# Performance work log

Measured on AMD Instinct MI355X. Metric: run time of the kernel, lower is better.

The kernel has to match this reference:

```python
import jax, jax.numpy as jnp
import numpy as np

N = 300000
H = 700
W_GRID = 700
CIN = 64
COUT = 64
K = 9


def setup_inputs() -> dict:
    rng = np.random.default_rng(0)
    lin = rng.permutation(H * W_GRID)[:N]
    ys = (lin // W_GRID).astype(np.int64)
    xs = (lin % W_GRID).astype(np.int64)
    grid = np.full(H * W_GRID, -1, np.int32)
    grid[lin] = np.arange(N, dtype=np.int32)
    offs = [(dy, dx) for dy in (-1, 0, 1) for dx in (-1, 0, 1)]

    def build(d):
        nbr = np.full((K, N), -1, np.int32)
        for k, (dy, dx) in enumerate(offs):
            ny = ys + dy * d
            nx = xs + dx * d
            valid = (ny >= 0) & (ny < H) & (nx >= 0) & (nx < W_GRID)
            l = np.clip(ny * W_GRID + nx, 0, H * W_GRID - 1)
            nbr[k] = np.where(valid, grid[l], -1)
        return jnp.asarray(nbr)

    nbr_d1 = build(1)
    nbr_d2 = build(2)

    key = jax.random.key(0)
    ks = jax.random.split(key, 16)
    f32 = jnp.float32

    def bn(k, c):
        s = jax.random.uniform(k, (c,), f32, 0.5, 1.5)
        b = jax.random.normal(jax.random.fold_in(k, 1), (c,), f32) * 0.1
        return s, b

    features = jax.random.normal(ks[0], (N, CIN), f32)
    W1 = jax.random.normal(ks[1], (K, CIN, COUT), f32) * 0.05
    W2a = jax.random.normal(ks[2], (CIN, COUT // 2), f32) * 0.05
    W2b = jax.random.normal(ks[3], (K, COUT // 2, COUT), f32) * 0.05
    W3 = jax.random.normal(ks[4], (K, CIN, COUT), f32) * 0.05
    Wf = jax.random.normal(ks[5], (3 * COUT, COUT), f32) * 0.05
    A1_w = jax.random.normal(ks[6], (3 * COUT, COUT // 4), f32) * 0.1
    A1_b = jnp.zeros((COUT // 4,), f32)
    A2_w = jax.random.normal(ks[7], (COUT // 4, 3 * COUT), f32) * 0.1
    A2_b = jnp.zeros((3 * COUT,), f32)
    bn1_s, bn1_b = bn(ks[8], COUT)
    bn2a_s, bn2a_b = bn(ks[9], COUT // 2)
    bn2b_s, bn2b_b = bn(ks[10], COUT)
    bn3_s, bn3_b = bn(ks[11], COUT)
    bnf_s, bnf_b = bn(ks[12], COUT)

    return dict(features=features, W1=W1, bn1_s=bn1_s, bn1_b=bn1_b,
                W2a=W2a, bn2a_s=bn2a_s, bn2a_b=bn2a_b,
                W2b=W2b, bn2b_s=bn2b_s, bn2b_b=bn2b_b,
                W3=W3, bn3_s=bn3_s, bn3_b=bn3_b,
                A1_w=A1_w, A1_b=A1_b, A2_w=A2_w, A2_b=A2_b,
                Wf=Wf, bnf_s=bnf_s, bnf_b=bnf_b,
                nbr_d1=nbr_d1, nbr_d2=nbr_d2)


def _sconv(f, nbr, W):
    # f: [N, Cin], nbr: [K, N] (-1 = no neighbor), W: [K, Cin, Cout]
    mask = (nbr >= 0)[..., None]                      # [K, N, 1]
    g = jnp.where(mask, f[jnp.clip(nbr, 0)], 0.0)     # [K, N, Cin] gather
    return jnp.einsum('knc,kcd->nd', g, W)            # [N, Cout]


def _bnrelu(x, s, b):
    # inference-mode BatchNorm folded into affine scale/shift, then ReLU
    return jax.nn.relu(x * s + b)


def reference(features, W1, bn1_s, bn1_b, W2a, bn2a_s, bn2a_b, W2b, bn2b_s, bn2b_b,
              W3, bn3_s, bn3_b, A1_w, A1_b, A2_w, A2_b, Wf, bnf_s, bnf_b,
              nbr_d1, nbr_d2):
    # path 1: 3x3 sparse conv + BN + ReLU
    feat1 = _bnrelu(_sconv(features, nbr_d1, W1), bn1_s, bn1_b)
    # path 2: 1x1 bottleneck + 3x3 sparse conv
    h = _bnrelu(features @ W2a, bn2a_s, bn2a_b)
    feat2 = _bnrelu(_sconv(h, nbr_d1, W2b), bn2b_s, bn2b_b)
    # path 3: 3x3 dilated (d=2) sparse conv
    feat3 = _bnrelu(_sconv(features, nbr_d2, W3), bn3_s, bn3_b)
    ms = jnp.concatenate([feat1, feat2, feat3], axis=1)   # [N, 3*Cout]
    # SE-style attention from global max pool over active sites
    pooled = jnp.max(ms, axis=0)                          # [3*Cout]
    attn = jax.nn.sigmoid(jax.nn.relu(pooled @ A1_w + A1_b) @ A2_w + A2_b)
    ms = ms * attn
    # 1x1 fusion conv + BN + ReLU
    fused = _bnrelu(ms @ Wf, bnf_s, bnf_b)                # [N, Cout]
    return fused
```

## Files before the change

### kernel.cpp

```cpp
#include <hip/hip_runtime.h>

#define N_PTS 300000
#define NPAD  300032
#define ZROW  N_PTS

typedef _Float16 f16;
typedef _Float16 f16x8 __attribute__((ext_vector_type(8)));
typedef float    f32x4 __attribute__((ext_vector_type(4)));

__device__ __forceinline__ f16 f2h(float x) { return (f16)x; }

union u4f16 { uint4 u; f16x8 h; };

#define HEAD_BLOCKS (NPAD / 256)
#define WP_BLOCKS   368

__global__ __launch_bounds__(256) void k_head(
    const float* __restrict__ feat, const float* __restrict__ W2a,
    const float* __restrict__ s2a, const float* __restrict__ b2a,
    const float* __restrict__ W1, const float* __restrict__ W2b,
    const float* __restrict__ W3,
    f16* __restrict__ featf, f16* __restrict__ hf,
    f16* __restrict__ Wt1, f16* __restrict__ Wt2b, f16* __restrict__ Wt3)
{
    if (blockIdx.x >= HEAD_BLOCKS) {
        int j = (blockIdx.x - HEAD_BLOCKS) * 256 + threadIdx.x;
        if (j < 36864) {
            int k = j >> 12, rem = j & 4095, d = rem >> 6, c = rem & 63;
            Wt1[j] = f2h(W1[(k << 12) + (c << 6) + d]);
        } else if (j < 73728) {
            int jj = j - 36864;
            int k = jj >> 12, rem = jj & 4095, d = rem >> 6, c = rem & 63;
            Wt3[jj] = f2h(W3[(k << 12) + (c << 6) + d]);
        } else if (j < 73728 + 18432) {
            int jj = j - 73728;
            int k = jj >> 11, rem = jj & 2047, d = rem >> 5, c2 = rem & 31;
            Wt2b[jj] = f2h(W2b[k * 2048 + c2 * 64 + d]);
        }
        return;
    }

    int lane = threadIdx.x & 63, wave = threadIdx.x >> 6;
    int n0 = (blockIdx.x * 4 + wave) * 64;
    int ln = lane & 15, q = lane >> 4;

    f16x8 a[4][2];
#pragma unroll
    for (int mt = 0; mt < 4; mt++) {
        int n = n0 + mt * 16 + ln;
#pragma unroll
        for (int ks = 0; ks < 2; ks++) {
            u4f16 v;
            if (n < N_PTS) {
                const float* p = feat + (long)n * 64 + ks * 32 + q * 8;
                float4 lo = *(const float4*)p;
                float4 hi = *(const float4*)(p + 4);
                v.h[0] = f2h(lo.x); v.h[1] = f2h(lo.y);
                v.h[2] = f2h(lo.z); v.h[3] = f2h(lo.w);
                v.h[4] = f2h(hi.x); v.h[5] = f2h(hi.y);
                v.h[6] = f2h(hi.z); v.h[7] = f2h(hi.w);
            } else {
                v.u = make_uint4(0u, 0u, 0u, 0u);
            }
            a[mt][ks] = v.h;
            *(uint4*)(featf + (long)n * 64 + ks * 32 + q * 8) = v.u;
        }
    }

    f32x4 acc[4][2];
    for (int mt = 0; mt < 4; mt++) for (int nt = 0; nt < 2; nt++)
        acc[mt][nt] = (f32x4){0.f, 0.f, 0.f, 0.f};
#pragma unroll
    for (int ks = 0; ks < 2; ks++)
#pragma unroll
        for (int nt = 0; nt < 2; nt++) {
            f16x8 b;
#pragma unroll
            for (int j = 0; j < 8; j++)
                b[j] = f2h(W2a[(ks * 32 + q * 8 + j) * 32 + nt * 16 + ln]);
#pragma unroll
            for (int mt = 0; mt < 4; mt++)
                acc[mt][nt] = __builtin_amdgcn_mfma_f32_16x16x32_f16(a[mt][ks], b, acc[mt][nt], 0, 0, 0);
        }

#pragma unroll
    for (int nt = 0; nt < 2; nt++) {
        int ch = nt * 16 + ln;
        float s = s2a[ch], bb = b2a[ch];
#pragma unroll
        for (int mt = 0; mt < 4; mt++)
#pragma unroll
            for (int r = 0; r < 4; r++) {
                int n = n0 + mt * 16 + q * 4 + r;
                float v = (n < N_PTS) ? fmaxf(acc[mt][nt][r] * s + bb, 0.f) : 0.f;
                hf[(long)n * 32 + ch] = f2h(v);
            }
    }
}

template <int CIN>
__device__ __forceinline__ void loadrows(
    uint4 (&dst)[4][CIN / 32], const int (&idx)[4],
    const f16* __restrict__ src, int q)
{
#pragma unroll
    for (int mt = 0; mt < 4; mt++) {
        const f16* p = src + (long)idx[mt] * CIN + q * 8;
#pragma unroll
        for (int ks = 0; ks < CIN / 32; ks++)
            dst[mt][ks] = *(const uint4*)(p + ks * 32);
    }
}

__device__ __forceinline__ void loadidx(
    int (&dst)[4], const int* __restrict__ nbr, int k, int n0, int ln)
{
    const int* nb = nbr + k * N_PTS;
#pragma unroll
    for (int mt = 0; mt < 4; mt++) {
        int nn = n0 + mt * 16 + ln;
        int v = (nn < N_PTS) ? nb[nn] : -1;
        dst[mt] = (v < 0) ? ZROW : v;
    }
}

template <int CIN>
__device__ __forceinline__ void conv_path(
    const f16* __restrict__ src, const f16* __restrict__ Wt,
    const int* __restrict__ nbr,
    int lane, int n0,
    const float* __restrict__ bns, const float* __restrict__ bnb,
    f16* __restrict__ msf, int colBase, float* __restrict__ pooled)
{
    constexpr int KS = CIN / 32;
    int ln = lane & 15, q = lane >> 4;

    f32x4 acc[4][4];
    for (int mt = 0; mt < 4; mt++) for (int nt = 0; nt < 4; nt++)
        acc[mt][nt] = (f32x4){0.f, 0.f, 0.f, 0.f};

    int  idxr[4][4];
    uint4 raw[4][4][KS];

#pragma unroll
    for (int k = 0; k < 4; k++) loadidx(idxr[k], nbr, k, n0, ln);
#pragma unroll
    for (int k = 0; k < 3; k++) loadrows<CIN>(raw[k], idxr[k], src, q);

#pragma unroll
    for (int k = 0; k < 9; k++) {
        if (k + 3 < 9) loadrows<CIN>(raw[(k + 3) & 3], idxr[(k + 3) & 3], src, q);
        if (k + 4 < 9) loadidx(idxr[k & 3], nbr, k + 4, n0, ln);
        const f16* Wk = Wt + k * CIN * 64;
#pragma unroll
        for (int ks = 0; ks < KS; ks++)
#pragma unroll
            for (int nt = 0; nt < 4; nt++) {
                f16x8 b = *(const f16x8*)(Wk + ((nt * 16 + ln) * CIN + ks * 32 + q * 8));
#pragma unroll
                for (int mt = 0; mt < 4; mt++) {
                    u4f16 v; v.u = raw[k & 3][mt][ks];
                    acc[mt][nt] = __builtin_amdgcn_mfma_f32_16x16x32_f16(v.h, b, acc[mt][nt], 0, 0, 0);
                }
            }
    }

#pragma unroll
    for (int nt = 0; nt < 4; nt++) {
        int ch = colBase + nt * 16 + ln;
        float s = bns[nt * 16 + ln], bb = bnb[nt * 16 + ln];
        float cmax = 0.f;
#pragma unroll
        for (int mt = 0; mt < 4; mt++)
#pragma unroll
            for (int r = 0; r < 4; r++) {
                int n = n0 + mt * 16 + q * 4 + r;
                float v = fmaxf(acc[mt][nt][r] * s + bb, 0.f);
                msf[(long)n * 192 + ch] = f2h(v);
                if (n < N_PTS) cmax = fmaxf(cmax, v);
            }
        cmax = fmaxf(cmax, __shfl_xor(cmax, 16));
        cmax = fmaxf(cmax, __shfl_xor(cmax, 32));
        if (q == 0) atomicMax((int*)(pooled + ch), __float_as_int(cmax));
    }
}

__global__ __launch_bounds__(256, 2) void k_conv(
    const f16* __restrict__ featf, const f16* __restrict__ hf,
    const f16* __restrict__ Wt1, const f16* __restrict__ Wt2b, const f16* __restrict__ Wt3,
    const int* __restrict__ nbr1, const int* __restrict__ nbr2,
    const float* __restrict__ bn1_s, const float* __restrict__ bn1_b,
    const float* __restrict__ bn2b_s, const float* __restrict__ bn2b_b,
    const float* __restrict__ bn3_s, const float* __restrict__ bn3_b,
    f16* __restrict__ msf, float* __restrict__ pooled)
{
    int lane = threadIdx.x & 63, wave = threadIdx.x >> 6;
    int u = blockIdx.x * 4 + wave;
    int tile = u / 3, path = u - tile * 3;
    int n0 = tile * 64;
    if (path == 0)
        conv_path<64>(featf, Wt1,  nbr1, lane, n0, bn1_s,  bn1_b,  msf, 0,   pooled);
    else if (path == 1)
        conv_path<32>(hf,    Wt2b, nbr1, lane, n0, bn2b_s, bn2b_b, msf, 64,  pooled);
    else
        conv_path<64>(featf, Wt3,  nbr2, lane, n0, bn3_s,  bn3_b,  msf, 128, pooled);
}

__global__ __launch_bounds__(256) void k_attn(
    const float* __restrict__ pooled,
    const float* __restrict__ A1w, const float* __restrict__ A1b,
    const float* __restrict__ A2w, const float* __restrict__ A2b,
    const float* __restrict__ Wf, f16* __restrict__ Wfst)
{
    __shared__ float sp[192], sa1[16], sattn[192];
    int t = threadIdx.x;
    if (t < 192) sp[t] = pooled[t];
    __syncthreads();
    if (t < 16) {
        float acc = A1b[t];
        for (int i = 0; i < 192; i++) acc += sp[i] * A1w[i * 16 + t];
        sa1[t] = fmaxf(acc, 0.f);
    }
    __syncthreads();
    if (t < 192) {
        float acc = A2b[t];
        for (int i = 0; i < 16; i++) acc += sa1[i] * A2w[i * 192 + t];
        sattn[t] = 1.f / (1.f + expf(-acc));
    }
    __syncthreads();
    for (int i = t; i < 192 * 64; i += 256) {
        int d = i / 192, j = i % 192;
        Wfst[i] = f2h(Wf[j * 64 + d] * sattn[j]);
    }
}

__global__ __launch_bounds__(256, 4) void k_fuse(
    const f16* __restrict__ msf, const f16* __restrict__ Wfst,
    const float* __restrict__ sf, const float* __restrict__ bf_,
    float* __restrict__ out)
{
    int lane = threadIdx.x & 63, wave = threadIdx.x >> 6;
    int n0 = (blockIdx.x * 4 + wave) * 32;
    int ln = lane & 15, q = lane >> 4;

    uint4 araw[6][2];
#pragma unroll
    for (int kt = 0; kt < 6; kt++)
#pragma unroll
        for (int mt = 0; mt < 2; mt++)
            araw[kt][mt] = *(const uint4*)(msf + (long)(n0 + mt * 16 + ln) * 192 + kt * 32 + q * 8);

    f32x4 acc[2][4];
    for (int mt = 0; mt < 2; mt++) for (int nt = 0; nt < 4; nt++)
        acc[mt][nt] = (f32x4){0.f, 0.f, 0.f, 0.f};

#pragma unroll
    for (int kt = 0; kt < 6; kt++)
#pragma unroll
        for (int nt = 0; nt < 4; nt++) {
            f16x8 b = *(const f16x8*)(Wfst + ((nt * 16 + ln) * 192 + kt * 32 + q * 8));
#pragma unroll
            for (int mt = 0; mt < 2; mt++) {
                u4f16 v; v.u = araw[kt][mt];
                acc[mt][nt] = __builtin_amdgcn_mfma_f32_16x16x32_f16(v.h, b, acc[mt][nt], 0, 0, 0);
            }
        }

#pragma unroll
    for (int nt = 0; nt < 4; nt++) {
        int ch = nt * 16 + ln;
        float s = sf[ch], bb = bf_[ch];
#pragma unroll
        for (int mt = 0; mt < 2; mt++)
#pragma unroll
            for (int r = 0; r < 4; r++) {
                int n = n0 + mt * 16 + q * 4 + r;
                if (n < N_PTS)
                    out[(long)n * 64 + ch] = fmaxf(acc[mt][nt][r] * s + bb, 0.f);
            }
    }
}

extern "C" void kernel_launch(void* const* d_in, const int* in_sizes, int n_in,
                              void* d_out, int out_size, void* d_ws, size_t ws_size,
                              hipStream_t stream)
{
    const float* features = (const float*)d_in[0];
    const float* W1     = (const float*)d_in[1];
    const float* bn1_s  = (const float*)d_in[2];
    const float* bn1_b  = (const float*)d_in[3];
    const float* W2a    = (const float*)d_in[4];
    const float* bn2a_s = (const float*)d_in[5];
    const float* bn2a_b = (const float*)d_in[6];
    const float* W2b    = (const float*)d_in[7];
    const float* bn2b_s = (const float*)d_in[8];
    const float* bn2b_b = (const float*)d_in[9];
    const float* W3     = (const float*)d_in[10];
    const float* bn3_s  = (const float*)d_in[11];
    const float* bn3_b  = (const float*)d_in[12];
    const float* A1w    = (const float*)d_in[13];
    const float* A1b    = (const float*)d_in[14];
    const float* A2w    = (const float*)d_in[15];
    const float* A2b    = (const float*)d_in[16];
    const float* Wf     = (const float*)d_in[17];
    const float* bnf_s  = (const float*)d_in[18];
    const float* bnf_b  = (const float*)d_in[19];
    const int*   nbr1   = (const int*)d_in[20];
    const int*   nbr2   = (const int*)d_in[21];

    char* ws = (char*)d_ws;
    size_t off = 0;
    f16* featf = (f16*)(ws + off); off += (size_t)NPAD * 64 * 2;
    f16* hf    = (f16*)(ws + off); off += (size_t)NPAD * 32 * 2;
    f16* msf   = (f16*)(ws + off); off += (size_t)NPAD * 192 * 2;
    f16* Wt1   = (f16*)(ws + off); off += 9 * 64 * 64 * 2;
    f16* Wt3   = (f16*)(ws + off); off += 9 * 64 * 64 * 2;
    f16* Wt2b  = (f16*)(ws + off); off += 9 * 32 * 64 * 2;
    f16* Wfst  = (f16*)(ws + off); off += 192 * 64 * 2;
    float* pooled = (float*)(ws + off); off += 256 * 4;

    hipMemsetAsync(pooled, 0, 192 * sizeof(float), stream);

    k_head<<<HEAD_BLOCKS + WP_BLOCKS, 256, 0, stream>>>(
        features, W2a, bn2a_s, bn2a_b, W1, W2b, W3,
        featf, hf, Wt1, Wt2b, Wt3);
    k_conv<<<(NPAD / 64) * 3 / 4, 256, 0, stream>>>(featf, hf, Wt1, Wt2b, Wt3, nbr1, nbr2,
                                           bn1_s, bn1_b, bn2b_s, bn2b_b, bn3_s, bn3_b,
                                           msf, pooled);
    k_attn<<<1, 256, 0, stream>>>(pooled, A1w, A1b, A2w, A2b, Wf, Wfst);
    k_fuse<<<NPAD / 128, 256, 0, stream>>>(msf, Wfst, bnf_s, bnf_b, (float*)d_out);
}
```

Measured before the change: 483.1 us.

## Hold conv weights in registers, swap MFMA operands, bpermute neighbor indices

The conv path now loads all 9 taps of weight fragments into registers up front instead of reloading them from memory per tap. It swaps the MFMA operand order so output channels map to rows, which lets each lane write 4 packed fp16 values per point and reduce the pooled max with lane shuffles. Neighbor indices are loaded once per lane for all taps and spread across lanes with ds_bpermute, and the gather ring shrinks to 3 slots. The much higher register use forces launch bounds down to 1 block per SM, which lowers occupancy and risks spilling.

```diff
diff --git a/kernel.cpp b/kernel.cpp
--- a/kernel.cpp
+++ b/kernel.cpp
@@ -99,28 +99,17 @@
 }
 
 template <int CIN>
-__device__ __forceinline__ void loadrows(
-    uint4 (&dst)[4][CIN / 32], const int (&idx)[4],
-    const f16* __restrict__ src, int q)
-{
-#pragma unroll
-    for (int mt = 0; mt < 4; mt++) {
-        const f16* p = src + (long)idx[mt] * CIN + q * 8;
+__device__ __forceinline__ void fill_tap(
+    uint4 (&slot)[4][CIN / 32], int idxk,
+    const f16* __restrict__ src, int ln, int q)
+{
+#pragma unroll
+    for (int pg = 0; pg < 4; pg++) {
+        int rid = __builtin_amdgcn_ds_bpermute((pg * 16 + ln) * 4, idxk);
+        const f16* p = src + (long)rid * CIN + q * 8;
 #pragma unroll
         for (int ks = 0; ks < CIN / 32; ks++)
-            dst[mt][ks] = *(const uint4*)(p + ks * 32);
-    }
-}
-
-__device__ __forceinline__ void loadidx(
-    int (&dst)[4], const int* __restrict__ nbr, int k, int n0, int ln)
-{
-    const int* nb = nbr + k * N_PTS;
-#pragma unroll
-    for (int mt = 0; mt < 4; mt++) {
-        int nn = n0 + mt * 16 + ln;
-        int v = (nn < N_PTS) ? nb[nn] : -1;
-        dst[mt] = (v < 0) ? ZROW : v;
+            slot[pg][ks] = *(const uint4*)(p + ks * 32);
     }
 }
 
@@ -135,57 +124,80 @@
     constexpr int KS = CIN / 32;
     int ln = lane & 15, q = lane >> 4;
 
+    int idxf[9];
+#pragma unroll
+    for (int k = 0; k < 9; k++) {
+        int nn = n0 + lane;
+        int v = (nn < N_PTS) ? nbr[k * N_PTS + nn] : -1;
+        idxf[k] = (v < 0) ? ZROW : v;
+    }
+
+    f16x8 wfr[9][4][KS];
+#pragma unroll
+    for (int t = 0; t < 9; t++)
+#pragma unroll
+        for (int ct = 0; ct < 4; ct++)
+#pragma unroll
+            for (int ks = 0; ks < KS; ks++)
+                wfr[t][ct][ks] = *(const f16x8*)(Wt + (t * 64 + ct * 16 + ln) * CIN + ks * 32 + q * 8);
+
     f32x4 acc[4][4];
-    for (int mt = 0; mt < 4; mt++) for (int nt = 0; nt < 4; nt++)
-        acc[mt][nt] = (f32x4){0.f, 0.f, 0.f, 0.f};
-
-    int  idxr[4][4];
-    uint4 raw[4][4][KS];
-
-#pragma unroll
-    for (int k = 0; k < 4; k++) loadidx(idxr[k], nbr, k, n0, ln);
-#pragma unroll
-    for (int k = 0; k < 3; k++) loadrows<CIN>(raw[k], idxr[k], src, q);
+    for (int ct = 0; ct < 4; ct++) for (int pg = 0; pg < 4; pg++)
+        acc[ct][pg] = (f32x4){0.f, 0.f, 0.f, 0.f};
+
+    uint4 ring[3][4][KS];
+    fill_tap<CIN>(ring[0], idxf[0], src, ln, q);
+    fill_tap<CIN>(ring[1], idxf[1], src, ln, q);
+    fill_tap<CIN>(ring[2], idxf[2], src, ln, q);
 
 #pragma unroll
     for (int k = 0; k < 9; k++) {
-        if (k + 3 < 9) loadrows<CIN>(raw[(k + 3) & 3], idxr[(k + 3) & 3], src, q);
-        if (k + 4 < 9) loadidx(idxr[k & 3], nbr, k + 4, n0, ln);
-        const f16* Wk = Wt + k * CIN * 64;
+        const int s = k % 3;
 #pragma unroll
         for (int ks = 0; ks < KS; ks++)
 #pragma unroll
-            for (int nt = 0; nt < 4; nt++) {
-                f16x8 b = *(const f16x8*)(Wk + ((nt * 16 + ln) * CIN + ks * 32 + q * 8));
-#pragma unroll
-                for (int mt = 0; mt < 4; mt++) {
-                    u4f16 v; v.u = raw[k & 3][mt][ks];
-                    acc[mt][nt] = __builtin_amdgcn_mfma_f32_16x16x32_f16(v.h, b, acc[mt][nt], 0, 0, 0);
+            for (int ct = 0; ct < 4; ct++)
+#pragma unroll
+                for (int pg = 0; pg < 4; pg++) {
+                    u4f16 v; v.u = ring[s][pg][ks];
+                    acc[ct][pg] = __builtin_amdgcn_mfma_f32_16x16x32_f16(
+                        wfr[k][ct][ks], v.h, acc[ct][pg], 0, 0, 0);
                 }
-            }
-    }
-
-#pragma unroll
-    for (int nt = 0; nt < 4; nt++) {
-        int ch = colBase + nt * 16 + ln;
-        float s = bns[nt * 16 + ln], bb = bnb[nt * 16 + ln];
-        float cmax = 0.f;
-#pragma unroll
-        for (int mt = 0; mt < 4; mt++)
+        if (k + 3 < 9) fill_tap<CIN>(ring[s], idxf[k + 3], src, ln, q);
+    }
+
+#pragma unroll
+    for (int ct = 0; ct < 4; ct++) {
+        f32x4 sv = *(const f32x4*)(bns + ct * 16 + q * 4);
+        f32x4 bv = *(const f32x4*)(bnb + ct * 16 + q * 4);
+        float rmax[4] = {0.f, 0.f, 0.f, 0.f};
+#pragma unroll
+        for (int pg = 0; pg < 4; pg++) {
+            int pt = n0 + pg * 16 + ln;
+            bool valid = pt < N_PTS;
+            union { f16 h[4]; uint2 u2; } pk;
 #pragma unroll
             for (int r = 0; r < 4; r++) {
-                int n = n0 + mt * 16 + q * 4 + r;
-                float v = fmaxf(acc[mt][nt][r] * s + bb, 0.f);
-                msf[(long)n * 192 + ch] = f2h(v);
-                if (n < N_PTS) cmax = fmaxf(cmax, v);
-            }
-        cmax = fmaxf(cmax, __shfl_xor(cmax, 16));
-        cmax = fmaxf(cmax, __shfl_xor(cmax, 32));
-        if (q == 0) atomicMax((int*)(pooled + ch), __float_as_int(cmax));
-    }
-}
-
-__global__ __launch_bounds__(256, 2) void k_conv(
+                float v = fmaxf(acc[ct][pg][r] * sv[r] + bv[r], 0.f);
+                pk.h[r] = f2h(v);
+                if (valid) rmax[r] = fmaxf(rmax[r], v);
+            }
+            *(uint2*)(msf + (long)pt * 192 + colBase + ct * 16 + q * 4) = pk.u2;
+        }
+#pragma unroll
+        for (int r = 0; r < 4; r++) {
+            float m = rmax[r];
+            m = fmaxf(m, __shfl_xor(m, 1));
+            m = fmaxf(m, __shfl_xor(m, 2));
+            m = fmaxf(m, __shfl_xor(m, 4));
+            m = fmaxf(m, __shfl_xor(m, 8));
+            if (ln == 0)
+                atomicMax((int*)(pooled + colBase + ct * 16 + q * 4 + r), __float_as_int(m));
+        }
+    }
+}
+
+__global__ __launch_bounds__(256, 1) void k_conv(
     const f16* __restrict__ featf, const f16* __restrict__ hf,
     const f16* __restrict__ Wt1, const f16* __restrict__ Wt2b, const f16* __restrict__ Wt3,
     const int* __restrict__ nbr1, const int* __restrict__ nbr2,
```

After: 739.2 us. 1.53x slower.
